# Optimization experiments

Hardware: AMD Instinct MI355X
Metric: run time of the kernel (lower is better)

## Reference

```python
import jax, jax.numpy as jnp
import numpy as np

N_NODES = 50000
N_EDGES = 1600000
IN_SIZE = 256
HIDDEN = 16
HEADS = 8
OUT_SIZE = 16
NEG_SLOPE = 0.2


def setup_inputs() -> dict:
    key = jax.random.key(0)
    ks = jax.random.split(key, 12)
    node_feat = jax.random.normal(ks[0], (N_NODES, IN_SIZE), dtype=jnp.float32)
    src = jax.random.randint(ks[1], (N_EDGES,), 0, N_NODES)
    dst = jax.random.randint(ks[2], (N_EDGES,), 0, N_NODES)
    d1 = HEADS * HIDDEN  # 128
    W1 = jax.random.normal(ks[3], (IN_SIZE, d1), dtype=jnp.float32) / np.sqrt(IN_SIZE)
    al1 = jax.random.normal(ks[4], (HEADS, HIDDEN), dtype=jnp.float32) / np.sqrt(HIDDEN)
    ar1 = jax.random.normal(ks[5], (HEADS, HIDDEN), dtype=jnp.float32) / np.sqrt(HIDDEN)
    b1 = jnp.zeros((d1,), dtype=jnp.float32)
    W2 = jax.random.normal(ks[6], (d1, HEADS * OUT_SIZE), dtype=jnp.float32) / np.sqrt(d1)
    al2 = jax.random.normal(ks[7], (HEADS, OUT_SIZE), dtype=jnp.float32) / np.sqrt(OUT_SIZE)
    ar2 = jax.random.normal(ks[8], (HEADS, OUT_SIZE), dtype=jnp.float32) / np.sqrt(OUT_SIZE)
    b2 = jnp.zeros((HEADS * OUT_SIZE,), dtype=jnp.float32)
    return {"node_feat": node_feat, "src": src, "dst": dst,
            "W1": W1, "al1": al1, "ar1": ar1, "b1": b1,
            "W2": W2, "al2": al2, "ar2": ar2, "b2": b2}


def _gat_conv(h, src, dst, W, attn_l, attn_r, bias, num_nodes):
    """DGL GATConv (eval mode, no dropout, no residual). Returns [N, H, D]."""
    H, D = attn_l.shape
    feat = (h @ W).reshape(-1, H, D)            # [N, H, D]
    el = jnp.sum(feat * attn_l, axis=-1)         # [N, H]
    er = jnp.sum(feat * attn_r, axis=-1)         # [N, H]
    e = jax.nn.leaky_relu(el[src] + er[dst], NEG_SLOPE)   # [E, H]
    # segment softmax over incoming edges of each dst node
    m = jax.ops.segment_max(e, dst, num_segments=num_nodes)
    m = jnp.where(jnp.isfinite(m), m, 0.0)       # guard isolated nodes
    ex = jnp.exp(e - m[dst])
    denom = jax.ops.segment_sum(ex, dst, num_segments=num_nodes)
    alpha = ex / denom[dst]                      # [E, H]
    msg = alpha[:, :, None] * feat[src]          # [E, H, D]
    out = jax.ops.segment_sum(msg, dst, num_segments=num_nodes)  # [N, H, D]
    return out + bias.reshape(H, D)


def reference(node_feat, src, dst, W1, al1, ar1, b1, W2, al2, ar2, b2):
    h = _gat_conv(node_feat, src, dst, W1, al1, ar1, b1, N_NODES)
    h = jax.nn.elu(h).reshape(N_NODES, -1)       # flatten(1) after activation
    out = _gat_conv(h, src, dst, W2, al2, ar2, b2, N_NODES)
    return out.mean(axis=1)                      # mean over heads -> [N, out_size]
```

## Files before the change

kernel.cpp:

```cpp
#include <hip/hip_runtime.h>
#include <hip/hip_bf16.h>

#define N_NODES 50000
#define N_EDGES 1600000
#define HEADS 8
#define HDIM 16
#define D1 128
#define NEG_SLOPE 0.2f
#define SCAN_BLKS 196
#define RTILES 3125

typedef short short8 __attribute__((ext_vector_type(8)));
typedef float f32x4 __attribute__((ext_vector_type(4)));
typedef _Float16 half2v __attribute__((ext_vector_type(2)));
typedef _Float16 half8 __attribute__((ext_vector_type(8)));

__device__ __forceinline__ float bf2f(ushort u) {
    union { unsigned u; float f; } x; x.u = ((unsigned)u) << 16; return x.f;
}
__device__ __forceinline__ ushort f2bf(float f) {
    union { float f; unsigned u; } x; x.f = f;
    unsigned r = x.u + 0x7FFF + ((x.u >> 16) & 1);
    return (ushort)(r >> 16);
}
__device__ __forceinline__ float ldf(const void* p, size_t i, int isf32) {
    return isf32 ? ((const float*)p)[i] : bf2f(((const ushort*)p)[i]);
}
__device__ __forceinline__ void splitbf(float f, ushort& hi, ushort& lo) {
    unsigned u = __float_as_uint(f);
    unsigned uh = u & 0xFFFF0000u;
    hi = (ushort)(uh >> 16);
    lo = f2bf(f - __uint_as_float(uh));
}

#define O_ROWPTR   0
#define O_DEG      200064
#define O_BSUM     400128
#define O_TMPSCAN  402176
#define O_FLAGS    602240
#define O_POS      602496
#define O_ESRC     2202624
#define O_W1HI     5402624
#define O_W1LO     5476352
#define O_W2HI     5550080
#define O_W2LO     5586944
#define O_B1F      5623808
#define O_B2F      5624320
#define O_FEATG    5624832
#define O_EL       18424832
#define O_ER       20024832
#define O_FEATG2   21624832
#define O_EL2      34424832
#define O_ER2      36024832


__device__ __forceinline__ void detect_body(const ushort* w1, int* flags, int* sm) {
    int t = threadIdx.x;
    int cnt = 0;
    for (int i = t; i < 32768; i += 256) {
        int e = (w1[i] >> 7) & 0xFF;
        if (e >= 0xC8) cnt++;
    }
    sm[t] = cnt; __syncthreads();
    for (int off = 128; off > 0; off >>= 1) {
        if (t < off) sm[t] += sm[t + off];
        __syncthreads();
    }
    if (t == 0) flags[0] = (sm[0] > 0) ? 1 : 0;
}

__global__ __launch_bounds__(256) void k_zerodetect(const ushort* __restrict__ w1,
                                                    int* __restrict__ deg, int* __restrict__ flags) {
    __shared__ int sm[256];
    int b = blockIdx.x;
    if (b < SCAN_BLKS) {
        int i = b * 256 + threadIdx.x;
        if (i < N_NODES) deg[i] = 0;
    } else {
        detect_body(w1, flags, sm);
    }
}

__device__ __forceinline__ void wprep_elem(const void* W, const void* al, const void* ar,
                                           int K, int kshift, ushort* whi, ushort* wlo,
                                           int isf32, int idx) {
    if (idx >= 144 * K) return;
    int n = idx >> kshift, k = idx & (K - 1);
    float f;
    if (n < 128) {
        f = ldf(W, (size_t)k * 128 + n, isf32);
    } else if (n < 136) {
        int h = n - 128;
        f = 0.f;
#pragma unroll
        for (int d = 0; d < HDIM; ++d)
            f = fmaf(ldf(W, (size_t)k * 128 + h * 16 + d, isf32), ldf(al, h * 16 + d, isf32), f);
    } else {
        int h = n - 136;
        f = 0.f;
#pragma unroll
        for (int d = 0; d < HDIM; ++d)
            f = fmaf(ldf(W, (size_t)k * 128 + h * 16 + d, isf32), ldf(ar, h * 16 + d, isf32), f);
    }
    ushort hi = f2bf(f);
    wlo[n * K + k] = f2bf(f - bf2f(hi));
    whi[n * K + k] = hi;
}

__global__ __launch_bounds__(256) void k_wprep(const void* __restrict__ W1, const void* __restrict__ al1,
                                               const void* __restrict__ ar1, const void* __restrict__ b1,
                                               const void* __restrict__ W2, const void* __restrict__ al2,
                                               const void* __restrict__ ar2, const void* __restrict__ b2,
                                               ushort* __restrict__ w1hi, ushort* __restrict__ w1lo,
                                               ushort* __restrict__ w2hi, ushort* __restrict__ w2lo,
                                               float* __restrict__ b1f, float* __restrict__ b2f,
                                               const int* __restrict__ flags) {
    int isf32 = flags[0];
    int u = blockIdx.x, t = threadIdx.x;
    if (u < 144) {
        wprep_elem(W1, al1, ar1, 256, 8, w1hi, w1lo, isf32, u * 256 + t);
    } else if (u < 216) {
        wprep_elem(W2, al2, ar2, 128, 7, w2hi, w2lo, isf32, (u - 144) * 256 + t);
    } else {
        if (t < 128) b1f[t] = ldf(b1, t, isf32);
        else b2f[t - 128] = ldf(b2, t - 128, isf32);
    }
}

__global__ __launch_bounds__(256) void k_scan1(const int* __restrict__ deg, int* __restrict__ tmp,
                                               int* __restrict__ bsum) {
    __shared__ int sm[256];
    int t = threadIdx.x;
    int i = blockIdx.x * 256 + t;
    int x = (i < N_NODES) ? deg[i] : 0;
    sm[t] = x; __syncthreads();
    for (int off = 1; off < 256; off <<= 1) {
        int v = (t >= off) ? sm[t - off] : 0;
        __syncthreads();
        sm[t] += v;
        __syncthreads();
    }
    if (i < N_NODES) tmp[i] = sm[t];
    if (t == 255) bsum[blockIdx.x] = sm[255];
}

__global__ __launch_bounds__(256) void k_scan23(const int* __restrict__ tmp, const int* __restrict__ bsum,
                                                int* __restrict__ rowptr) {
    __shared__ int sm[256];
    int t = threadIdx.x;
    int x = (t < SCAN_BLKS) ? bsum[t] : 0;
    sm[t] = x; __syncthreads();
    for (int off = 1; off < 256; off <<= 1) {
        int v = (t >= off) ? sm[t - off] : 0;
        __syncthreads();
        sm[t] += v;
        __syncthreads();
    }
    int boff = sm[blockIdx.x] - ((blockIdx.x < SCAN_BLKS) ? bsum[blockIdx.x] : 0);
    int i = blockIdx.x * 256 + t;
    if (i < N_NODES) rowptr[i + 1] = tmp[i] + boff;
    if (i == 0) rowptr[0] = 0;
}

__device__ __forceinline__ void store_tile(_Float16 (*sfe)[72], _Float16* featg,
                                           const f32x4* acc, int lane, int quad, int l16,
                                           int rowb0, int cbase) {
#pragma unroll
    for (int ci = 0; ci < 4; ++ci)
#pragma unroll
        for (int r = 0; r < 4; ++r)
            sfe[quad * 4 + r][ci * 16 + l16] = (_Float16)acc[ci][r];
    int rr = lane >> 3, ch = lane & 7;
#pragma unroll
    for (int s = 0; s < 2; ++s) {
        int row = s * 8 + rr;
        short8 v = *(const short8*)&sfe[row][ch * 8];
        *(short8*)(featg + (size_t)(rowb0 + row) * D1 + cbase * 16 + ch * 8) = v;
    }
}

__device__ __forceinline__ void gemm1_wave9(const void* A, const ushort* Bhi, const ushort* Blo,
                                            _Float16* featg, float* el, float* er,
                                            int isf32, int rt, int lane, _Float16 (*sfe)[72]) {
    int quad = lane >> 4, l16 = lane & 15;
    const int K = 256;
    size_t a_off = (size_t)(rt * 16 + l16) * K + quad * 8;
    int rowb0 = rt * 16;

    short8 ahi[8], alo[8];
    if (isf32) {
        const float* ap = (const float*)A + a_off;
#pragma unroll
        for (int i = 0; i < 8; ++i) {
            f32x4 u0 = *(const f32x4*)(ap + 32 * i);
            f32x4 u1 = *(const f32x4*)(ap + 32 * i + 4);
            float a8[8] = {u0[0], u0[1], u0[2], u0[3], u1[0], u1[1], u1[2], u1[3]};
#pragma unroll
            for (int j = 0; j < 8; ++j) {
                ushort h, l;
                splitbf(a8[j], h, l);
                ahi[i][j] = (short)h; alo[i][j] = (short)l;
            }
        }
    } else {
        const ushort* ap = (const ushort*)A + a_off;
#pragma unroll
        for (int i = 0; i < 8; ++i) ahi[i] = *(const short8*)(ap + 32 * i);
    }

#pragma unroll
    for (int g = 0; g < 2; ++g) {
        f32x4 acc[4];
#pragma unroll
        for (int ci = 0; ci < 4; ++ci) acc[ci] = (f32x4){0.f, 0.f, 0.f, 0.f};
#pragma unroll
        for (int ci = 0; ci < 4; ++ci) {
            int c = g * 4 + ci;
            const ushort* bh = Bhi + (size_t)(c * 16 + l16) * K + quad * 8;
            if (isf32) {
                const ushort* bl = Blo + (size_t)(c * 16 + l16) * K + quad * 8;
#pragma unroll
                for (int k = 0; k < 8; ++k) {
                    short8 bh8 = *(const short8*)(bh + 32 * k);
                    short8 bl8 = *(const short8*)(bl + 32 * k);
                    acc[ci] = __builtin_amdgcn_mfma_f32_16x16x32_bf16(ahi[k], bh8, acc[ci], 0, 0, 0);
                    acc[ci] = __builtin_amdgcn_mfma_f32_16x16x32_bf16(ahi[k], bl8, acc[ci], 0, 0, 0);
                    acc[ci] = __builtin_amdgcn_mfma_f32_16x16x32_bf16(alo[k], bh8, acc[ci], 0, 0, 0);
                }
            } else {
#pragma unroll
                for (int k = 0; k < 8; ++k) {
                    short8 bh8 = *(const short8*)(bh + 32 * k);
                    acc[ci] = __builtin_amdgcn_mfma_f32_16x16x32_bf16(ahi[k], bh8, acc[ci], 0, 0, 0);
                }
            }
        }
        store_tile(sfe, featg, acc, lane, quad, l16, rowb0, g * 4);
    }

    {
        const ushort* bh = Bhi + (size_t)(8 * 16 + l16) * K + quad * 8;
        const ushort* bl = Blo + (size_t)(8 * 16 + l16) * K + quad * 8;
        f32x4 a = {0.f, 0.f, 0.f, 0.f};
#pragma unroll
        for (int k = 0; k < 8; ++k) {
            short8 bh8 = *(const short8*)(bh + 32 * k);
            short8 bl8 = *(const short8*)(bl + 32 * k);
            a = __builtin_amdgcn_mfma_f32_16x16x32_bf16(ahi[k], bh8, a, 0, 0, 0);
            a = __builtin_amdgcn_mfma_f32_16x16x32_bf16(ahi[k], bl8, a, 0, 0, 0);
            if (isf32) a = __builtin_amdgcn_mfma_f32_16x16x32_bf16(alo[k], bh8, a, 0, 0, 0);
        }
#pragma unroll
        for (int r = 0; r < 4; ++r) {
            int row = rowb0 + quad * 4 + r;
            if (l16 < 8) el[row * 8 + l16] = a[r];
            else         er[row * 8 + (l16 - 8)] = a[r];
        }
    }
}

__global__ __launch_bounds__(256) void k_countgemm1(const int4* __restrict__ dst4, int* __restrict__ deg,
                                                    uchar4* __restrict__ pos4,
                                                    const void* __restrict__ A,
                                                    const ushort* __restrict__ w1hi, const ushort* __restrict__ w1lo,
                                                    _Float16* __restrict__ featg,
                                                    float* __restrict__ el, float* __restrict__ er,
                                                    const int* __restrict__ flags) {
    __shared__ __align__(16) _Float16 sfe[4][16][72];
    int b = blockIdx.x, t = threadIdx.x;
    if (!(b & 1)) {
        int i = (b >> 1) * 256 + t;
        if (i < N_EDGES / 4) {
            int4 d = dst4[i];
            uchar4 p;
            p.x = (unsigned char)atomicAdd(&deg[d.x], 1);
            p.y = (unsigned char)atomicAdd(&deg[d.y], 1);
            p.z = (unsigned char)atomicAdd(&deg[d.z], 1);
            p.w = (unsigned char)atomicAdd(&deg[d.w], 1);
            pos4[i] = p;
        }
    } else {
        int g = b >> 1;
        if (g < 782) {
            int wave = t >> 6, lane = t & 63;
            int rt = g * 4 + wave;
            if (rt < RTILES)
                gemm1_wave9(A, w1hi, w1lo, featg, el, er, flags[0], rt, lane, sfe[wave]);
        }
    }
}

__global__ __launch_bounds__(256) void k_place(const int4* __restrict__ src4, const int4* __restrict__ dst4,
                                               const int* __restrict__ rowptr, const uchar4* __restrict__ pos4,
                                               ushort* __restrict__ esrc) {
    int i = blockIdx.x * 256 + threadIdx.x;
    if (i < N_EDGES / 4) {
        int4 s = src4[i], d = dst4[i];
        uchar4 p = pos4[i];
        esrc[rowptr[d.x] + p.x] = (ushort)s.x;
        esrc[rowptr[d.y] + p.y] = (ushort)s.y;
        esrc[rowptr[d.z] + p.z] = (ushort)s.z;
        esrc[rowptr[d.w] + p.w] = (ushort)s.w;
    }
}

__device__ __forceinline__ void gather_wide(const int* __restrict__ rowptr, const ushort* __restrict__ esrc,
                                            const _Float16* __restrict__ featg,
                                            const float* __restrict__ el, const float* __restrict__ er,
                                            int v, int lane, float (&acc)[8], float& den, int& deg) {
    int h8 = lane & 7, esel = lane >> 3;
    int part = lane & 15, a = lane >> 4, hpart = part >> 1;
    float erv = er[v * 8 + h8];
    int beg = rowptr[v], end = rowptr[v + 1];
    deg = end - beg;
#pragma unroll
    for (int c = 0; c < 8; ++c) acc[c] = 0.f;
    den = 0.f;
    for (int j = beg; j < end; j += 8) {
        int nv = end - j;
        int idx = j + h8; if (idx >= end) idx = end - 1;
        int sv = (int)esrc[idx];
        int se = __shfl(sv, esel);
        float x = el[se * 8 + h8] + erv;
        x = x > 0.f ? x : NEG_SLOPE * x;
        float w = __expf(x);
        if (esel >= nv) w = 0.f;
        int s0 = __shfl(sv, a);
        int s1 = __shfl(sv, a + 4);
        half8 g0 = *(const half8*)(featg + (size_t)s0 * 128 + part * 8);
        half8 g1 = *(const half8*)(featg + (size_t)s1 * 128 + part * 8);
        float w0 = __shfl(w, a * 8 + hpart);
        float w1 = __shfl(w, (a + 4) * 8 + hpart);
        den += w0 + w1;
#pragma unroll
        for (int c = 0; c < 8; ++c)
            acc[c] = fmaf(w0, (float)g0[c], fmaf(w1, (float)g1[c], acc[c]));
    }
#pragma unroll
    for (int c = 0; c < 8; ++c) {
        acc[c] += __shfl_xor(acc[c], 16);
        acc[c] += __shfl_xor(acc[c], 32);
    }
    den += __shfl_xor(den, 16);
    den += __shfl_xor(den, 32);
}

__global__ __launch_bounds__(256) void k_agg1m(const int* __restrict__ rowptr, const ushort* __restrict__ esrc,
                                               const _Float16* __restrict__ featg,
                                               const float* __restrict__ el, const float* __restrict__ er,
                                               const float* __restrict__ b1f,
                                               const ushort* __restrict__ w2hi, const ushort* __restrict__ w2lo,
                                               _Float16* __restrict__ featg2,
                                               float* __restrict__ el2, float* __restrict__ er2,
                                               const int* __restrict__ flags) {
    __shared__ __align__(16) ushort sh_hi[16][136];
    __shared__ __align__(16) ushort sh_lo[16][136];
    int isf32 = flags[0];
    int wave = threadIdx.x >> 6, lane = threadIdx.x & 63;
    int part = lane & 15, a = lane >> 4;
    int vb = blockIdx.x * 16;
    f32x4 bia0 = *(const f32x4*)(b1f + part * 8);
    f32x4 bia1 = *(const f32x4*)(b1f + part * 8 + 4);
#pragma unroll
    for (int i = 0; i < 4; ++i) {
        int v = vb + wave * 4 + i;
        float acc[8], den; int dg;
        gather_wide(rowptr, esrc, featg, el, er, v, lane, acc, den, dg);
        float inv = (dg > 0) ? 1.0f / den : 0.f;
        if (a == 0) {
            short8 hi8, lo8;
#pragma unroll
            for (int c = 0; c < 8; ++c) {
                float bc = (c < 4) ? bia0[c] : bia1[c - 4];
                float r = fmaf(acc[c], inv, bc);
                r = r > 0.f ? r : (__expf(r) - 1.f);
                ushort h, l;
                splitbf(r, h, l);
                hi8[c] = (short)h; lo8[c] = (short)l;
            }
            int m = wave * 4 + i;
            *(short8*)&sh_hi[m][part * 8] = hi8;
            *(short8*)&sh_lo[m][part * 8] = lo8;
        }
    }
    __syncthreads();

    int quad = lane >> 4, l16 = lane & 15;
    const int K = 128;
    short8 ahi[4], alo[4];
#pragma unroll
    for (int k = 0; k < 4; ++k) {
        ahi[k] = *(const short8*)&sh_hi[l16][quad * 8 + 32 * k];
        alo[k] = *(const short8*)&sh_lo[l16][quad * 8 + 32 * k];
    }
    int ntile = (wave == 0) ? 3 : 2;
    for (int ti = 0; ti < ntile; ++ti) {
        int c = (ti == 2) ? 8 : wave + ti * 4;
        const ushort* bh = w2hi + (size_t)(c * 16 + l16) * K + quad * 8;
        const ushort* bl = w2lo + (size_t)(c * 16 + l16) * K + quad * 8;
        f32x4 aa = {0.f, 0.f, 0.f, 0.f};
#pragma unroll
        for (int k = 0; k < 4; ++k) {
            short8 bh8 = *(const short8*)(bh + 32 * k);
            aa = __builtin_amdgcn_mfma_f32_16x16x32_bf16(ahi[k], bh8, aa, 0, 0, 0);
            aa = __builtin_amdgcn_mfma_f32_16x16x32_bf16(alo[k], bh8, aa, 0, 0, 0);
            if (c == 8 || isf32) {
                short8 bl8 = *(const short8*)(bl + 32 * k);
                aa = __builtin_amdgcn_mfma_f32_16x16x32_bf16(ahi[k], bl8, aa, 0, 0, 0);
            }
        }
        if (c < 8) {
#pragma unroll
            for (int r = 0; r < 4; ++r)
                featg2[(size_t)(vb + quad * 4 + r) * D1 + c * 16 + l16] = (_Float16)aa[r];
        } else {
#pragma unroll
            for (int r = 0; r < 4; ++r) {
                int row = vb + quad * 4 + r;
                if (l16 < 8) el2[row * 8 + l16] = aa[r];
                else         er2[row * 8 + (l16 - 8)] = aa[r];
            }
        }
    }
}

__global__ __launch_bounds__(256) void k_agg2(const int* __restrict__ rowptr, const ushort* __restrict__ esrc,
                                              const _Float16* __restrict__ featg2,
                                              const float* __restrict__ el2, const float* __restrict__ er2,
                                              const float* __restrict__ b2f,
                                              void* __restrict__ out, const int* __restrict__ flags) {
    int wave = threadIdx.x >> 6, lane = threadIdx.x & 63;
    int v = blockIdx.x * 4 + wave;
    if (v >= N_NODES) return;
    int part = lane & 15;
    float acc[8], den; int dg;
    gather_wide(rowptr, esrc, featg2, el2, er2, v, lane, acc, den, dg);
    float inv = (dg > 0) ? 1.0f / den : 0.f;
    f32x4 bia0 = *(const f32x4*)(b2f + part * 8);
    f32x4 bia1 = *(const f32x4*)(b2f + part * 8 + 4);
    float r[8];
#pragma unroll
    for (int c = 0; c < 8; ++c) {
        float bc = (c < 4) ? bia0[c] : bia1[c - 4];
        r[c] = fmaf(acc[c], inv, bc);
    }
#pragma unroll
    for (int c = 0; c < 8; ++c) {
        r[c] += __shfl_xor(r[c], 2);
        r[c] += __shfl_xor(r[c], 4);
        r[c] += __shfl_xor(r[c], 8);
        r[c] *= 0.125f;
    }
    if (lane < 2) {
        if (flags[0]) {
            float* op = (float*)out + (size_t)v * 16 + lane * 8;
            f32x4 o0 = {r[0], r[1], r[2], r[3]};
            f32x4 o1 = {r[4], r[5], r[6], r[7]};
            *(f32x4*)op = o0;
            *(f32x4*)(op + 4) = o1;
        } else {
            short8 pk;
#pragma unroll
            for (int c = 0; c < 8; ++c) pk[c] = (short)f2bf(r[c]);
            *(short8*)((ushort*)out + (size_t)v * 16 + lane * 8) = pk;
        }
    }
}

extern "C" void kernel_launch(void* const* d_in, const int* in_sizes, int n_in,
                              void* d_out, int out_size, void* d_ws, size_t ws_size,
                              hipStream_t stream) {
    const void* node_feat = d_in[0];
    const int4* src4 = (const int4*)d_in[1];
    const int4* dst4 = (const int4*)d_in[2];
    const void* W1 = d_in[3];
    const void* al1 = d_in[4];
    const void* ar1 = d_in[5];
    const void* b1 = d_in[6];
    const void* W2 = d_in[7];
    const void* al2 = d_in[8];
    const void* ar2 = d_in[9];
    const void* b2 = d_in[10];
    char* ws = (char*)d_ws;

    int* rowptr = (int*)(ws + O_ROWPTR);
    int* deg    = (int*)(ws + O_DEG);
    int* bsum   = (int*)(ws + O_BSUM);
    int* tmpsc  = (int*)(ws + O_TMPSCAN);
    int* flags  = (int*)(ws + O_FLAGS);
    uchar4* pos4 = (uchar4*)(ws + O_POS);
    ushort* esrc = (ushort*)(ws + O_ESRC);
    ushort* w1hi = (ushort*)(ws + O_W1HI);
    ushort* w1lo = (ushort*)(ws + O_W1LO);
    ushort* w2hi = (ushort*)(ws + O_W2HI);
    ushort* w2lo = (ushort*)(ws + O_W2LO);
    float* b1f  = (float*)(ws + O_B1F);
    float* b2f  = (float*)(ws + O_B2F);
    _Float16* featg = (_Float16*)(ws + O_FEATG);
    float* el   = (float*)(ws + O_EL);
    float* er   = (float*)(ws + O_ER);
    _Float16* featg2 = (_Float16*)(ws + O_FEATG2);
    float* el2  = (float*)(ws + O_EL2);
    float* er2  = (float*)(ws + O_ER2);

    k_zerodetect<<<SCAN_BLKS + 1, 256, 0, stream>>>((const ushort*)W1, deg, flags);
    k_wprep<<<217, 256, 0, stream>>>(W1, al1, ar1, b1, W2, al2, ar2, b2,
                                     w1hi, w1lo, w2hi, w2lo, b1f, b2f, flags);
    k_countgemm1<<<3126, 256, 0, stream>>>(dst4, deg, pos4, node_feat, w1hi, w1lo,
                                           featg, el, er, flags);
    k_scan1<<<SCAN_BLKS, 256, 0, stream>>>(deg, tmpsc, bsum);
    k_scan23<<<SCAN_BLKS, 256, 0, stream>>>(tmpsc, bsum, rowptr);
    k_place<<<1563, 256, 0, stream>>>(src4, dst4, rowptr, pos4, esrc);
    k_agg1m<<<N_NODES / 16, 256, 0, stream>>>(rowptr, esrc, featg, el, er, b1f,
                                              w2hi, w2lo, featg2, el2, er2, flags);
    k_agg2<<<(N_NODES + 3) / 4, 256, 0, stream>>>(rowptr, esrc, featg2, el2, er2,
                                                  b2f, d_out, flags);
}
```

Measured before the change: 423.7 us.

## Replace global-atomic degree counting with per-block LDS histograms and merged scan

Counting in-degrees now happens in 128 blocks, each building a packed 16-bit LDS histogram over its slice of edges, instead of issuing global atomics per edge. A merge kernel computes per-block base offsets and total degrees, so the old zeroing pass is dropped and the placement adds a per-block base. The layer-1 GEMM moves from the counting kernel into the placement kernel so it still overlaps with edge work. The per-block histograms use 8-bit counts and offsets, which assumes small per-node degrees, and the merge pass adds about 12.8 MB of extra histogram traffic.

Result: faster. 394.4 us (-6.9%).

```diff
diff --git a/kernel.cpp b/kernel.cpp
--- a/kernel.cpp
+++ b/kernel.cpp
@@ -9,11 +9,13 @@
 #define NEG_SLOPE 0.2f
 #define SCAN_BLKS 196
 #define RTILES 3125
+#define NHB 128
+#define EPB4 3125
 
 typedef short short8 __attribute__((ext_vector_type(8)));
 typedef float f32x4 __attribute__((ext_vector_type(4)));
-typedef _Float16 half2v __attribute__((ext_vector_type(2)));
 typedef _Float16 half8 __attribute__((ext_vector_type(8)));
+typedef unsigned char uchar;
 
 __device__ __forceinline__ float bf2f(ushort u) {
     union { unsigned u; float f; } x; x.u = ((unsigned)u) << 16; return x.f;
@@ -52,9 +54,12 @@
 #define O_FEATG2   21624832
 #define O_EL2      34424832
 #define O_ER2      36024832
-
-
-__device__ __forceinline__ void detect_body(const ushort* w1, int* flags, int* sm) {
+#define O_HISTG    O_FEATG2
+#define O_BLKBASE  (O_FEATG2 + 6400000)
+
+
+__global__ __launch_bounds__(256) void k_detect(const ushort* __restrict__ w1, int* __restrict__ flags) {
+    __shared__ int sm[256];
     int t = threadIdx.x;
     int cnt = 0;
     for (int i = t; i < 32768; i += 256) {
@@ -67,18 +72,6 @@
         __syncthreads();
     }
     if (t == 0) flags[0] = (sm[0] > 0) ? 1 : 0;
-}
-
-__global__ __launch_bounds__(256) void k_zerodetect(const ushort* __restrict__ w1,
-                                                    int* __restrict__ deg, int* __restrict__ flags) {
-    __shared__ int sm[256];
-    int b = blockIdx.x;
-    if (b < SCAN_BLKS) {
-        int i = b * 256 + threadIdx.x;
-        if (i < N_NODES) deg[i] = 0;
-    } else {
-        detect_body(w1, flags, sm);
-    }
 }
 
 __device__ __forceinline__ void wprep_elem(const void* W, const void* al, const void* ar,
@@ -127,6 +120,45 @@
     }
 }
 
+__global__ __launch_bounds__(256) void k_hist(const int4* __restrict__ dst4,
+                                              uchar* __restrict__ histU, uchar4* __restrict__ pos4) {
+    __shared__ uint hh[25000];
+    int b = blockIdx.x, t = threadIdx.x;
+    for (int w = t; w < 25000; w += 256) hh[w] = 0;
+    __syncthreads();
+    int base = b * EPB4;
+    for (int j = t; j < EPB4; j += 256) {
+        int4 d = dst4[base + j];
+        uchar4 p;
+        { int w = d.x >> 1, sh = (d.x & 1) << 4; p.x = (uchar)(__atomic_fetch_add((unsigned*)&hh[w], 1u << sh, __ATOMIC_RELAXED) >> sh); }
+        { int w = d.y >> 1, sh = (d.y & 1) << 4; p.y = (uchar)(__atomic_fetch_add((unsigned*)&hh[w], 1u << sh, __ATOMIC_RELAXED) >> sh); }
+        { int w = d.z >> 1, sh = (d.z & 1) << 4; p.z = (uchar)(__atomic_fetch_add((unsigned*)&hh[w], 1u << sh, __ATOMIC_RELAXED) >> sh); }
+        { int w = d.w >> 1, sh = (d.w & 1) << 4; p.w = (uchar)(__atomic_fetch_add((unsigned*)&hh[w], 1u << sh, __ATOMIC_RELAXED) >> sh); }
+        pos4[base + j] = p;
+    }
+    __syncthreads();
+    ushort* out = (ushort*)(histU + (size_t)b * 50000);
+    for (int w = t; w < 25000; w += 256) {
+        uint v = hh[w];
+        out[w] = (ushort)((v & 0xFF) | ((v >> 8) & 0xFF00));
+    }
+}
+
+__global__ __launch_bounds__(256) void k_scanmerge(const uchar* __restrict__ histU,
+                                                   uchar* __restrict__ bb, int* __restrict__ deg) {
+    int n = blockIdx.x * 256 + threadIdx.x;
+    if (n >= N_NODES) return;
+    int run = 0;
+#pragma unroll 8
+    for (int b = 0; b < NHB; ++b) {
+        size_t idx = (size_t)b * 50000 + n;
+        int c = histU[idx];
+        bb[idx] = (uchar)run;
+        run += c;
+    }
+    deg[n] = run;
+}
+
 __global__ __launch_bounds__(256) void k_scan1(const int* __restrict__ deg, int* __restrict__ tmp,
                                                int* __restrict__ bsum) {
     __shared__ int sm[256];
@@ -259,8 +291,10 @@
     }
 }
 
-__global__ __launch_bounds__(256) void k_countgemm1(const int4* __restrict__ dst4, int* __restrict__ deg,
-                                                    uchar4* __restrict__ pos4,
+__global__ __launch_bounds__(256) void k_placegemm1(const int4* __restrict__ src4, const int4* __restrict__ dst4,
+                                                    const int* __restrict__ rowptr, const uchar4* __restrict__ pos4,
+                                                    const uchar* __restrict__ bb,
+                                                    ushort* __restrict__ esrc,
                                                     const void* __restrict__ A,
                                                     const ushort* __restrict__ w1hi, const ushort* __restrict__ w1lo,
                                                     _Float16* __restrict__ featg,
@@ -268,39 +302,22 @@
                                                     const int* __restrict__ flags) {
     __shared__ __align__(16) _Float16 sfe[4][16][72];
     int b = blockIdx.x, t = threadIdx.x;
-    if (!(b & 1)) {
-        int i = (b >> 1) * 256 + t;
+    if (b < 1563) {
+        int i = b * 256 + t;
         if (i < N_EDGES / 4) {
-            int4 d = dst4[i];
-            uchar4 p;
-            p.x = (unsigned char)atomicAdd(&deg[d.x], 1);
-            p.y = (unsigned char)atomicAdd(&deg[d.y], 1);
-            p.z = (unsigned char)atomicAdd(&deg[d.z], 1);
-            p.w = (unsigned char)atomicAdd(&deg[d.w], 1);
-            pos4[i] = p;
+            int4 s = src4[i], d = dst4[i];
+            uchar4 p = pos4[i];
+            const uchar* bbrow = bb + (size_t)(i / EPB4) * 50000;
+            esrc[rowptr[d.x] + bbrow[d.x] + p.x] = (ushort)s.x;
+            esrc[rowptr[d.y] + bbrow[d.y] + p.y] = (ushort)s.y;
+            esrc[rowptr[d.z] + bbrow[d.z] + p.z] = (ushort)s.z;
+            esrc[rowptr[d.w] + bbrow[d.w] + p.w] = (ushort)s.w;
         }
     } else {
-        int g = b >> 1;
-        if (g < 782) {
-            int wave = t >> 6, lane = t & 63;
-            int rt = g * 4 + wave;
-            if (rt < RTILES)
-                gemm1_wave9(A, w1hi, w1lo, featg, el, er, flags[0], rt, lane, sfe[wave]);
-        }
-    }
-}
-
-__global__ __launch_bounds__(256) void k_place(const int4* __restrict__ src4, const int4* __restrict__ dst4,
-                                               const int* __restrict__ rowptr, const uchar4* __restrict__ pos4,
-                                               ushort* __restrict__ esrc) {
-    int i = blockIdx.x * 256 + threadIdx.x;
-    if (i < N_EDGES / 4) {
-        int4 s = src4[i], d = dst4[i];
-        uchar4 p = pos4[i];
-        esrc[rowptr[d.x] + p.x] = (ushort)s.x;
-        esrc[rowptr[d.y] + p.y] = (ushort)s.y;
-        esrc[rowptr[d.z] + p.z] = (ushort)s.z;
-        esrc[rowptr[d.w] + p.w] = (ushort)s.w;
+        int wave = t >> 6, lane = t & 63;
+        int rt = (b - 1563) * 4 + wave;
+        if (rt < RTILES)
+            gemm1_wave9(A, w1hi, w1lo, featg, el, er, flags[0], rt, lane, sfe[wave]);
     }
 }
 
@@ -490,6 +507,8 @@
     int* flags  = (int*)(ws + O_FLAGS);
     uchar4* pos4 = (uchar4*)(ws + O_POS);
     ushort* esrc = (ushort*)(ws + O_ESRC);
+    uchar* histU = (uchar*)(ws + O_HISTG);
+    uchar* bbase = (uchar*)(ws + O_BLKBASE);
     ushort* w1hi = (ushort*)(ws + O_W1HI);
     ushort* w1lo = (ushort*)(ws + O_W1LO);
     ushort* w2hi = (ushort*)(ws + O_W2HI);
@@ -503,14 +522,15 @@
     float* el2  = (float*)(ws + O_EL2);
     float* er2  = (float*)(ws + O_ER2);
 
-    k_zerodetect<<<SCAN_BLKS + 1, 256, 0, stream>>>((const ushort*)W1, deg, flags);
+    k_detect<<<1, 256, 0, stream>>>((const ushort*)W1, flags);
     k_wprep<<<217, 256, 0, stream>>>(W1, al1, ar1, b1, W2, al2, ar2, b2,
                                      w1hi, w1lo, w2hi, w2lo, b1f, b2f, flags);
-    k_countgemm1<<<3126, 256, 0, stream>>>(dst4, deg, pos4, node_feat, w1hi, w1lo,
-                                           featg, el, er, flags);
+    k_hist<<<NHB, 256, 0, stream>>>(dst4, histU, pos4);
+    k_scanmerge<<<SCAN_BLKS, 256, 0, stream>>>(histU, bbase, deg);
     k_scan1<<<SCAN_BLKS, 256, 0, stream>>>(deg, tmpsc, bsum);
     k_scan23<<<SCAN_BLKS, 256, 0, stream>>>(tmpsc, bsum, rowptr);
-    k_place<<<1563, 256, 0, stream>>>(src4, dst4, rowptr, pos4, esrc);
+    k_placegemm1<<<1563 + 782, 256, 0, stream>>>(src4, dst4, rowptr, pos4, bbase, esrc,
+                                                 node_feat, w1hi, w1lo, featg, el, er, flags);
     k_agg1m<<<N_NODES / 16, 256, 0, stream>>>(rowptr, esrc, featg, el, er, b1f,
                                               w2hi, w2lo, featg2, el2, er2, flags);
     k_agg2<<<(N_NODES + 3) / 4, 256, 0, stream>>>(rowptr, esrc, featg2, el2, er2,
```

## Replace atomic-count CSR build with two-pass bucketed radix sort by destination

Applied to the files above, without the earlier changes.

Builds the destination-sorted edge list with a two-level bucket sort instead of a global per-node atomic degree count, a three-kernel scan and a scatter place pass. The first pass bins edges into 196 coarse buckets through shared-memory staging and writes packed (src, dst-low-byte) words. The second pass sorts each bucket locally in shared memory and emits rowptr and esrc with coalesced writes. This removes the per-edge global atomics, the random scatter and two launches. In exchange, bucket capacity is fixed at 12288, so heavily skewed degree distributions would overflow and drop edges, and the packed buffer reuses the featg2 workspace region.

New measurement: 362.8 us. -14.4%, faster.

```diff
diff --git a/kernel.cpp b/kernel.cpp
--- a/kernel.cpp
+++ b/kernel.cpp
@@ -7,13 +7,16 @@
 #define HDIM 16
 #define D1 128
 #define NEG_SLOPE 0.2f
-#define SCAN_BLKS 196
 #define RTILES 3125
+#define NB 196
+#define BCAP 12288
+#define B1BLK 125
+#define EPB1 12800
 
 typedef short short8 __attribute__((ext_vector_type(8)));
 typedef float f32x4 __attribute__((ext_vector_type(4)));
-typedef _Float16 half2v __attribute__((ext_vector_type(2)));
 typedef _Float16 half8 __attribute__((ext_vector_type(8)));
+typedef unsigned char uchar;
 
 __device__ __forceinline__ float bf2f(ushort u) {
     union { unsigned u; float f; } x; x.u = ((unsigned)u) << 16; return x.f;
@@ -34,11 +37,9 @@
 }
 
 #define O_ROWPTR   0
-#define O_DEG      200064
-#define O_BSUM     400128
-#define O_TMPSCAN  402176
+#define O_GCUR     200064
+#define O_BBASE    400128
 #define O_FLAGS    602240
-#define O_POS      602496
 #define O_ESRC     2202624
 #define O_W1HI     5402624
 #define O_W1LO     5476352
@@ -52,10 +53,17 @@
 #define O_FEATG2   21624832
 #define O_EL2      34424832
 #define O_ER2      36024832
-
-
-__device__ __forceinline__ void detect_body(const ushort* w1, int* flags, int* sm) {
+#define O_PKBUF    O_FEATG2
+
+
+__global__ __launch_bounds__(256) void k_detect(const ushort* __restrict__ w1, int* __restrict__ flags,
+                                                int* __restrict__ gcur) {
+    __shared__ int sm[256];
     int t = threadIdx.x;
+    if (blockIdx.x == 1) {
+        if (t < NB) gcur[t] = 0;
+        return;
+    }
     int cnt = 0;
     for (int i = t; i < 32768; i += 256) {
         int e = (w1[i] >> 7) & 0xFF;
@@ -67,18 +75,6 @@
         __syncthreads();
     }
     if (t == 0) flags[0] = (sm[0] > 0) ? 1 : 0;
-}
-
-__global__ __launch_bounds__(256) void k_zerodetect(const ushort* __restrict__ w1,
-                                                    int* __restrict__ deg, int* __restrict__ flags) {
-    __shared__ int sm[256];
-    int b = blockIdx.x;
-    if (b < SCAN_BLKS) {
-        int i = b * 256 + threadIdx.x;
-        if (i < N_NODES) deg[i] = 0;
-    } else {
-        detect_body(w1, flags, sm);
-    }
 }
 
 __device__ __forceinline__ void wprep_elem(const void* W, const void* al, const void* ar,
@@ -127,41 +123,6 @@
     }
 }
 
-__global__ __launch_bounds__(256) void k_scan1(const int* __restrict__ deg, int* __restrict__ tmp,
-                                               int* __restrict__ bsum) {
-    __shared__ int sm[256];
-    int t = threadIdx.x;
-    int i = blockIdx.x * 256 + t;
-    int x = (i < N_NODES) ? deg[i] : 0;
-    sm[t] = x; __syncthreads();
-    for (int off = 1; off < 256; off <<= 1) {
-        int v = (t >= off) ? sm[t - off] : 0;
-        __syncthreads();
-        sm[t] += v;
-        __syncthreads();
-    }
-    if (i < N_NODES) tmp[i] = sm[t];
-    if (t == 255) bsum[blockIdx.x] = sm[255];
-}
-
-__global__ __launch_bounds__(256) void k_scan23(const int* __restrict__ tmp, const int* __restrict__ bsum,
-                                                int* __restrict__ rowptr) {
-    __shared__ int sm[256];
-    int t = threadIdx.x;
-    int x = (t < SCAN_BLKS) ? bsum[t] : 0;
-    sm[t] = x; __syncthreads();
-    for (int off = 1; off < 256; off <<= 1) {
-        int v = (t >= off) ? sm[t - off] : 0;
-        __syncthreads();
-        sm[t] += v;
-        __syncthreads();
-    }
-    int boff = sm[blockIdx.x] - ((blockIdx.x < SCAN_BLKS) ? bsum[blockIdx.x] : 0);
-    int i = blockIdx.x * 256 + t;
-    if (i < N_NODES) rowptr[i + 1] = tmp[i] + boff;
-    if (i == 0) rowptr[0] = 0;
-}
-
 __device__ __forceinline__ void store_tile(_Float16 (*sfe)[72], _Float16* featg,
                                            const f32x4* acc, int lane, int quad, int l16,
                                            int rowb0, int cbase) {
@@ -259,49 +220,129 @@
     }
 }
 
-__global__ __launch_bounds__(256) void k_countgemm1(const int4* __restrict__ dst4, int* __restrict__ deg,
-                                                    uchar4* __restrict__ pos4,
-                                                    const void* __restrict__ A,
-                                                    const ushort* __restrict__ w1hi, const ushort* __restrict__ w1lo,
-                                                    _Float16* __restrict__ featg,
-                                                    float* __restrict__ el, float* __restrict__ er,
-                                                    const int* __restrict__ flags) {
-    __shared__ __align__(16) _Float16 sfe[4][16][72];
+__device__ __forceinline__ void block_scan(int* sm, int t) {
+    for (int off = 1; off < 256; off <<= 1) {
+        int v = (t >= off) ? sm[t - off] : 0;
+        __syncthreads();
+        sm[t] += v;
+        __syncthreads();
+    }
+}
+
+__global__ __launch_bounds__(256) void k_b1gemm1(const int4* __restrict__ src4, const int4* __restrict__ dst4,
+                                                 int* __restrict__ gcur, uint* __restrict__ pkbuf,
+                                                 const void* __restrict__ A,
+                                                 const ushort* __restrict__ w1hi, const ushort* __restrict__ w1lo,
+                                                 _Float16* __restrict__ featg,
+                                                 float* __restrict__ el, float* __restrict__ er,
+                                                 const int* __restrict__ flags) {
+    __shared__ __align__(16) char smem[54592];
     int b = blockIdx.x, t = threadIdx.x;
-    if (!(b & 1)) {
-        int i = (b >> 1) * 256 + t;
-        if (i < N_EDGES / 4) {
-            int4 d = dst4[i];
-            uchar4 p;
-            p.x = (unsigned char)atomicAdd(&deg[d.x], 1);
-            p.y = (unsigned char)atomicAdd(&deg[d.y], 1);
-            p.z = (unsigned char)atomicAdd(&deg[d.z], 1);
-            p.w = (unsigned char)atomicAdd(&deg[d.w], 1);
-            pos4[i] = p;
+    if (b < B1BLK) {
+        uint* stage = (uint*)smem;
+        uint* cnt   = (uint*)(smem + 51200);
+        int*  loff  = (int*)(smem + 51984);
+        int*  goff  = (int*)(smem + 52768);
+        int*  sm    = (int*)(smem + 53552);
+        for (int w = t; w < NB; w += 256) cnt[w] = 0;
+        __syncthreads();
+        int base4 = b * (EPB1 / 4);
+        for (int g = t; g < EPB1 / 4; g += 256) {
+            int4 d = dst4[base4 + g];
+            atomicAdd(&cnt[d.x >> 8], 1u);
+            atomicAdd(&cnt[d.y >> 8], 1u);
+            atomicAdd(&cnt[d.z >> 8], 1u);
+            atomicAdd(&cnt[d.w >> 8], 1u);
+        }
+        __syncthreads();
+        int c = (t < NB) ? (int)cnt[t] : 0;
+        sm[t] = c;
+        __syncthreads();
+        block_scan(sm, t);
+        if (t < NB) {
+            loff[t] = sm[t] - c;
+            goff[t] = atomicAdd(&gcur[t], c);
+            cnt[t] = 0;
+        }
+        __syncthreads();
+        for (int g = t; g < EPB1 / 4; g += 256) {
+            int4 s = src4[base4 + g];
+            int4 d = dst4[base4 + g];
+            { int bk = d.x >> 8; int r = atomicAdd(&cnt[bk], 1u); stage[loff[bk] + r] = ((uint)s.x << 8) | (uint)(d.x & 255); }
+            { int bk = d.y >> 8; int r = atomicAdd(&cnt[bk], 1u); stage[loff[bk] + r] = ((uint)s.y << 8) | (uint)(d.y & 255); }
+            { int bk = d.z >> 8; int r = atomicAdd(&cnt[bk], 1u); stage[loff[bk] + r] = ((uint)s.z << 8) | (uint)(d.z & 255); }
+            { int bk = d.w >> 8; int r = atomicAdd(&cnt[bk], 1u); stage[loff[bk] + r] = ((uint)s.w << 8) | (uint)(d.w & 255); }
+        }
+        __syncthreads();
+        for (int bk = 0; bk < NB; ++bk) {
+            int n = cnt[bk], lo = loff[bk], go = goff[bk];
+            for (int k = t; k < n; k += 256) {
+                int gi = go + k;
+                if (gi < BCAP) pkbuf[(size_t)bk * BCAP + gi] = stage[lo + k];
+            }
         }
     } else {
-        int g = b >> 1;
-        if (g < 782) {
-            int wave = t >> 6, lane = t & 63;
-            int rt = g * 4 + wave;
-            if (rt < RTILES)
-                gemm1_wave9(A, w1hi, w1lo, featg, el, er, flags[0], rt, lane, sfe[wave]);
-        }
-    }
-}
-
-__global__ __launch_bounds__(256) void k_place(const int4* __restrict__ src4, const int4* __restrict__ dst4,
-                                               const int* __restrict__ rowptr, const uchar4* __restrict__ pos4,
-                                               ushort* __restrict__ esrc) {
-    int i = blockIdx.x * 256 + threadIdx.x;
-    if (i < N_EDGES / 4) {
-        int4 s = src4[i], d = dst4[i];
-        uchar4 p = pos4[i];
-        esrc[rowptr[d.x] + p.x] = (ushort)s.x;
-        esrc[rowptr[d.y] + p.y] = (ushort)s.y;
-        esrc[rowptr[d.z] + p.z] = (ushort)s.z;
-        esrc[rowptr[d.w] + p.w] = (ushort)s.w;
-    }
+        int g = b - B1BLK;
+        _Float16 (*sfe4)[16][72] = (_Float16(*)[16][72])smem;
+        int wave = t >> 6, lane = t & 63;
+        int rt = g * 4 + wave;
+        if (rt < RTILES)
+            gemm1_wave9(A, w1hi, w1lo, featg, el, er, flags[0], rt, lane, sfe4[wave]);
+    }
+}
+
+__global__ __launch_bounds__(256) void k_bscan(const int* __restrict__ gcur, int* __restrict__ bbase,
+                                               int* __restrict__ rowptr) {
+    __shared__ int sm[256];
+    int t = threadIdx.x;
+    int x = (t < NB) ? gcur[t] : 0;
+    sm[t] = x;
+    __syncthreads();
+    block_scan(sm, t);
+    if (t == 0) bbase[0] = 0;
+    bbase[t + 1] = sm[t];
+    if (t == NB - 1) rowptr[N_NODES] = sm[t];
+}
+
+__global__ __launch_bounds__(256) void k_bucket2(const uint* __restrict__ pkbuf, const int* __restrict__ gcur,
+                                                 const int* __restrict__ bbase,
+                                                 ushort* __restrict__ esrc, int* __restrict__ rowptr) {
+    __shared__ __align__(16) char smem[76800];
+    uint*   pk    = (uint*)smem;
+    ushort* es    = (ushort*)(smem + 49152);
+    uint*   ncnt  = (uint*)(smem + 73728);
+    int*    nbase = (int*)(smem + 74752);
+    int*    sm    = (int*)(smem + 75776);
+    int b = blockIdx.x, t = threadIdx.x;
+    int nb = gcur[b]; if (nb > BCAP) nb = BCAP;
+    int bb0 = bbase[b];
+    ncnt[t] = 0;
+    __syncthreads();
+    for (int k = t; k < nb; k += 256) {
+        uint u = pkbuf[(size_t)b * BCAP + k];
+        pk[k] = u;
+        atomicAdd(&ncnt[u & 255u], 1u);
+    }
+    __syncthreads();
+    int c = (int)ncnt[t];
+    sm[t] = c;
+    __syncthreads();
+    block_scan(sm, t);
+    nbase[t] = sm[t] - c;
+    int v = b * 256 + t;
+    if (v < N_NODES) rowptr[v] = bb0 + sm[t] - c;
+    ncnt[t] = 0;
+    __syncthreads();
+    for (int k = t; k < nb; k += 256) {
+        uint u = pk[k];
+        int n = (int)(u & 255u);
+        int r = (int)atomicAdd(&ncnt[n], 1u);
+        int p = nbase[n] + r;
+        if (p < BCAP) es[p] = (ushort)(u >> 8);
+    }
+    __syncthreads();
+    for (int k = t; k < nb; k += 256)
+        esrc[bb0 + k] = es[k];
 }
 
 __device__ __forceinline__ void gather_wide(const int* __restrict__ rowptr, const ushort* __restrict__ esrc,
@@ -484,12 +525,11 @@
     char* ws = (char*)d_ws;
 
     int* rowptr = (int*)(ws + O_ROWPTR);
-    int* deg    = (int*)(ws + O_DEG);
-    int* bsum   = (int*)(ws + O_BSUM);
-    int* tmpsc  = (int*)(ws + O_TMPSCAN);
+    int* gcur   = (int*)(ws + O_GCUR);
+    int* bbase  = (int*)(ws + O_BBASE);
     int* flags  = (int*)(ws + O_FLAGS);
-    uchar4* pos4 = (uchar4*)(ws + O_POS);
     ushort* esrc = (ushort*)(ws + O_ESRC);
+    uint* pkbuf = (uint*)(ws + O_PKBUF);
     ushort* w1hi = (ushort*)(ws + O_W1HI);
     ushort* w1lo = (ushort*)(ws + O_W1LO);
     ushort* w2hi = (ushort*)(ws + O_W2HI);
@@ -503,14 +543,13 @@
     float* el2  = (float*)(ws + O_EL2);
     float* er2  = (float*)(ws + O_ER2);
 
-    k_zerodetect<<<SCAN_BLKS + 1, 256, 0, stream>>>((const ushort*)W1, deg, flags);
+    k_detect<<<2, 256, 0, stream>>>((const ushort*)W1, flags, gcur);
     k_wprep<<<217, 256, 0, stream>>>(W1, al1, ar1, b1, W2, al2, ar2, b2,
                                      w1hi, w1lo, w2hi, w2lo, b1f, b2f, flags);
-    k_countgemm1<<<3126, 256, 0, stream>>>(dst4, deg, pos4, node_feat, w1hi, w1lo,
-                                           featg, el, er, flags);
-    k_scan1<<<SCAN_BLKS, 256, 0, stream>>>(deg, tmpsc, bsum);
-    k_scan23<<<SCAN_BLKS, 256, 0, stream>>>(tmpsc, bsum, rowptr);
-    k_place<<<1563, 256, 0, stream>>>(src4, dst4, rowptr, pos4, esrc);
+    k_b1gemm1<<<B1BLK + 782, 256, 0, stream>>>(src4, dst4, gcur, pkbuf,
+                                               node_feat, w1hi, w1lo, featg, el, er, flags);
+    k_bscan<<<1, 256, 0, stream>>>(gcur, bbase, rowptr);
+    k_bucket2<<<NB, 256, 0, stream>>>(pkbuf, gcur, bbase, esrc, rowptr);
     k_agg1m<<<N_NODES / 16, 256, 0, stream>>>(rowptr, esrc, featg, el, er, b1f,
                                               w2hi, w2lo, featg2, el2, er2, flags);
     k_agg2<<<(N_NODES + 3) / 4, 256, 0, stream>>>(rowptr, esrc, featg2, el2, er2,
```
